# Kernel tuning notes

Hardware: AMD Instinct MI355X
Metric: run time of the kernel (lower is better)

## Reference

```python
import jax, jax.numpy as jnp
import numpy as np

NUM_CLASSES = 2
TOP_K = 200
CONF_THRESH = 0.01
NMS_THRESH = 0.45
VAR0, VAR1 = 0.1, 0.2
NUM_PRIORS = 72192
BATCH = 64


def setup_inputs() -> dict:
    key = jax.random.key(0)
    k1, k2, k3 = jax.random.split(key, 3)
    loc_data = jax.random.normal(k1, (BATCH, NUM_PRIORS, 4), dtype=jnp.float32)
    conf_data = jax.random.uniform(k2, (BATCH * NUM_PRIORS, NUM_CLASSES), dtype=jnp.float32)
    prior_data = jax.random.uniform(k3, (NUM_PRIORS, 4), dtype=jnp.float32) * 0.5 + 0.01
    return {"loc_data": loc_data, "conf_data": conf_data, "prior_data": prior_data}


def decode(loc, priors):
    # loc, priors: [P, 4] (cx, cy, w, h) -> corners (x1, y1, x2, y2)
    cxcy = priors[:, :2] + loc[:, :2] * VAR0 * priors[:, 2:]
    wh = priors[:, 2:] * jnp.exp(loc[:, 2:] * VAR1)
    return jnp.concatenate([cxcy - wh / 2, cxcy + wh / 2], axis=-1)


def pairwise_iou(boxes):
    # boxes: [K, 4] corners
    area = (boxes[:, 2] - boxes[:, 0]) * (boxes[:, 3] - boxes[:, 1])
    lt = jnp.maximum(boxes[:, None, :2], boxes[None, :, :2])
    rb = jnp.minimum(boxes[:, None, 2:], boxes[None, :, 2:])
    wh = jnp.clip(rb - lt, 0.0)
    inter = wh[..., 0] * wh[..., 1]
    union = area[:, None] + area[None, :] - inter
    return inter / jnp.maximum(union, 1e-12)


def nms_single(boxes, scores):
    # boxes: [P,4], scores: [P] -> [TOP_K, 5] rows (score, x1, y1, x2, y2)
    masked = jnp.where(scores > CONF_THRESH, scores, -jnp.inf)
    top_scores, idx = jax.lax.top_k(masked, TOP_K)      # descending, like torch nms
    cand_boxes = boxes[idx]                              # [K,4]
    valid = top_scores > CONF_THRESH
    iou = pairwise_iou(cand_boxes)                       # [K,K]
    ar = jnp.arange(TOP_K)

    def body(i, keep):
        sup = (iou[i] > NMS_THRESH) & (ar > i)
        return jnp.where(keep[i], keep & ~sup, keep)

    keep = jax.lax.fori_loop(0, TOP_K, body, valid)
    # compact kept detections to the front (matches output[i, cl, :count] = ...)
    pos = jnp.cumsum(keep) - 1
    pos = jnp.where(keep, pos, TOP_K)                    # dropped rows scatter out of range
    rows = jnp.concatenate([top_scores[:, None], cand_boxes], axis=1)
    return jnp.zeros((TOP_K, 5), dtype=boxes.dtype).at[pos].set(rows, mode="drop")


def reference(loc_data, conf_data, prior_data):
    num = loc_data.shape[0]
    num_priors = prior_data.shape[0]
    conf_preds = conf_data.reshape(num, num_priors, NUM_CLASSES)  # [B, P, C]
    decoded = jax.vmap(decode, in_axes=(0, None))(loc_data, prior_data)  # [B, P, 4]
    per_class = []
    # class 0 is background -> zeros (matches torch output init)
    per_class.append(jnp.zeros((num, TOP_K, 5), dtype=loc_data.dtype))
    for cl in range(1, NUM_CLASSES):
        per_class.append(jax.vmap(nms_single)(decoded, conf_preds[:, :, cl]))
    # final rank-based zeroing in torch source is a no-op (fill_ on an advanced-index copy)
    return jnp.stack(per_class, axis=1)  # [B, C, TOP_K, 5]
```

## Files before the change

kernel.cpp:

```cpp
#include <hip/hip_runtime.h>
#include <math.h>

#pragma clang fp contract(off)

#define NUM_PRIORS 72192
#define BATCH      64
#define TOPK       200
#define CONF_TH    0.01f
#define NMS_TH     0.45f
#define NBINS      256
#define SLICES     32
#define ROWS       (NUM_PRIORS / SLICES)
#define Q4         (ROWS / 2)
#define CAPS       64
#define CAP        1024
#define KW         7
#define NMS_NTH    1024

typedef unsigned long long u64;

__device__ __forceinline__ int bin_of(float s) {
    int b = (int)(s * 256.0f);
    return b > 255 ? 255 : b;
}

__global__ __launch_bounds__(256) void histcollect_kernel(const float* __restrict__ conf,
                                                          unsigned short* __restrict__ shist,
                                                          unsigned* __restrict__ scnt,
                                                          u64* __restrict__ cand) {
    __shared__ unsigned lh[4][NBINS];
    __shared__ unsigned lcnt;
    const int b = blockIdx.y, slice = blockIdx.x, tid = threadIdx.x;
    const int wv = tid >> 6;
    for (int i = tid; i < 4 * NBINS; i += 256) ((unsigned*)lh)[i] = 0;
    if (tid == 0) lcnt = 0;
    __syncthreads();
    const float4* c4 = (const float4*)conf;
    const long base4 = (long)b * (NUM_PRIORS / 2) + (long)slice * Q4;
    const int prow0 = slice * ROWS;
    u64* seg = cand + ((long)b * SLICES + slice) * CAPS;

    float4 v0 = c4[base4 + tid];
    float4 v1 = c4[base4 + tid + 256];
    float4 v2 = c4[base4 + tid + 512];
    float4 v3 = c4[base4 + tid + 768];

#define PROC(sv, pidx)                                                          \
    do {                                                                        \
        float s_ = (sv);                                                        \
        if (s_ > CONF_TH) {                                                     \
            int bn = bin_of(s_);                                                \
            atomicAdd(&lh[wv][bn], 1u);                                         \
            if (bn == 255) {                                                    \
                unsigned pos = atomicAdd(&lcnt, 1u);                            \
                if (pos < CAPS)                                                 \
                    seg[pos] = ((u64)__float_as_uint(s_) << 32) |               \
                               (u64)(0xFFFFFFFFu - (unsigned)(pidx));           \
            }                                                                   \
        }                                                                       \
    } while (0)

    PROC(v0.y, prow0 + 2 * tid);
    PROC(v0.w, prow0 + 2 * tid + 1);
    PROC(v1.y, prow0 + 2 * (tid + 256));
    PROC(v1.w, prow0 + 2 * (tid + 256) + 1);
    PROC(v2.y, prow0 + 2 * (tid + 512));
    PROC(v2.w, prow0 + 2 * (tid + 512) + 1);
    PROC(v3.y, prow0 + 2 * (tid + 768));
    PROC(v3.w, prow0 + 2 * (tid + 768) + 1);
    if (tid < Q4 - 1024) {
        float4 vt = c4[base4 + tid + 1024];
        PROC(vt.y, prow0 + 2 * (tid + 1024));
        PROC(vt.w, prow0 + 2 * (tid + 1024) + 1);
    }
#undef PROC
    __syncthreads();
    shist[((long)b * SLICES + slice) * NBINS + tid] =
        (unsigned short)(lh[0][tid] + lh[1][tid] + lh[2][tid] + lh[3][tid]);
    if (tid == 0) {
        unsigned c = lcnt;
        scnt[b * SLICES + slice] = (c < CAPS) ? c : CAPS;
    }
}

__global__ __launch_bounds__(256) void fixup_kernel(const float* __restrict__ conf,
                                                    const unsigned short* __restrict__ shist,
                                                    unsigned* __restrict__ scnt,
                                                    u64* __restrict__ cand) {
    __shared__ unsigned suf[NBINS];
    __shared__ int Tsh;
    __shared__ unsigned lcnt;
    const int b = blockIdx.x, tid = threadIdx.x;
    unsigned acc = 0;
    const unsigned short* hb = shist + (long)b * SLICES * NBINS;
#pragma unroll
    for (int s = 0; s < SLICES; s++) acc += (unsigned)hb[s * NBINS + tid];
    suf[tid] = acc;
    if (tid == 0) Tsh = 0;
    __syncthreads();
    for (int off = 1; off < NBINS; off <<= 1) {
        unsigned v = (tid + off < NBINS) ? suf[tid + off] : 0u;
        __syncthreads();
        suf[tid] += v;
        __syncthreads();
    }
    unsigned s0 = suf[tid];
    unsigned sn = (tid + 1 < NBINS) ? suf[tid + 1] : 0u;
    if (s0 >= TOPK && (tid == NBINS - 1 || sn < TOPK)) Tsh = tid;
    __syncthreads();
    const int T = Tsh;
    if (T == 255) return;

    const float4* c4 = (const float4*)conf;
    for (int s = 0; s < SLICES; s++) {
        __syncthreads();
        if (tid == 0) lcnt = 0;
        __syncthreads();
        const long base4 = (long)b * (NUM_PRIORS / 2) + (long)s * Q4;
        const int prow0 = s * ROWS;
        u64* seg = cand + ((long)b * SLICES + s) * CAPS;
        for (int q = tid; q < Q4; q += 256) {
            float4 v = c4[base4 + q];
            float sy = v.y, sw = v.w;
            if (sy > CONF_TH && bin_of(sy) >= T) {
                unsigned pos = atomicAdd(&lcnt, 1u);
                if (pos < CAPS)
                    seg[pos] = ((u64)__float_as_uint(sy) << 32) |
                               (u64)(0xFFFFFFFFu - (unsigned)(prow0 + 2 * q));
            }
            if (sw > CONF_TH && bin_of(sw) >= T) {
                unsigned pos = atomicAdd(&lcnt, 1u);
                if (pos < CAPS)
                    seg[pos] = ((u64)__float_as_uint(sw) << 32) |
                               (u64)(0xFFFFFFFFu - (unsigned)(prow0 + 2 * q + 1));
            }
        }
        __syncthreads();
        if (tid == 0) {
            unsigned c = lcnt;
            scnt[b * SLICES + s] = (c < CAPS) ? c : CAPS;
        }
    }
}

__global__ __launch_bounds__(NMS_NTH) void nms_kernel(const float* __restrict__ loc,
                           const float* __restrict__ prior,
                           const unsigned* __restrict__ scnt,
                           const u64* __restrict__ cand,
                           float* __restrict__ out) {
    __shared__ u64 keys[CAP];
    __shared__ float4 bbox[224];
    __shared__ float bsc_s[TOPK];
    __shared__ unsigned invR[TOPK][8];
    __shared__ unsigned kw0[8];
    __shared__ unsigned kwF[KW];
    __shared__ unsigned char vld[TOPK];
    __shared__ int soff[SLICES + 1];
    __shared__ int scl[SLICES];
    const int b = blockIdx.x, tid = threadIdx.x;

    if (tid < 64) {
        int s = tid;
        int c = 0;
        if (s < SLICES) {
            unsigned cs = scnt[b * SLICES + s];
            c = (cs < CAPS) ? (int)cs : CAPS;
        }
        int v = c;
#pragma unroll
        for (int d = 1; d < 32; d <<= 1) {
            int o = __shfl_up(v, d);
            if ((int)tid >= d) v += o;
        }
        if (s < SLICES) {
            int P = v - c;
            int off = P > CAP ? CAP : P;
            int rem = CAP - off;
            int cl = c < rem ? c : rem;
            soff[s] = off;
            scl[s] = cl;
            if (s == SLICES - 1) soff[SLICES] = (P + c > CAP) ? CAP : (P + c);
        }
    }
    {
        float* ob = out + (long)b * 2 * TOPK * 5;
        for (int i = tid; i < 2 * TOPK * 5; i += NMS_NTH) ob[i] = 0.f;
    }
    if (tid < 224) {
        bbox[tid] = make_float4(0.f, 0.f, 0.f, 0.f);
        if (tid < TOPK) { bsc_s[tid] = 0.f; vld[tid] = 0; }
    }
    __syncthreads();

    const int n = soff[SLICES];
    const int nn = (n + 15) & ~15;
    for (int pos = tid; pos < SLICES * CAPS; pos += NMS_NTH) {
        int s = pos >> 6, idx = pos & 63;
        if (idx < scl[s])
            keys[soff[s] + idx] = cand[((long)b * SLICES + s) * CAPS + idx];
    }
    for (int i = n + tid; i < nn; i += NMS_NTH) keys[i] = 0ull;
    __syncthreads();

    u64 kc = (tid < n) ? keys[tid] : 0ull;
    int rk = 0;
    if ((int)(tid & ~63u) < n) {
        for (int k = 0; k < nn; k += 16) {
            u64 kb[16];
#pragma unroll
            for (int j = 0; j < 16; j++) kb[j] = keys[k + j];
#pragma unroll
            for (int j = 0; j < 16; j++) rk += (kb[j] > kc) ? 1 : 0;
        }
    }
    if (tid < n && rk < TOPK) {
        u64 key = kc;
        float sc = __uint_as_float((unsigned)(key >> 32));
        unsigned p = 0xFFFFFFFFu - (unsigned)(key & 0xFFFFFFFFull);
        float4 l4 = ((const float4*)loc)[(long)b * NUM_PRIORS + p];
        float4 p4 = ((const float4*)prior)[p];
        float cx = p4.x + (l4.x * 0.1f) * p4.z;
        float cy = p4.y + (l4.y * 0.1f) * p4.w;
        float w_ = p4.z * (float)exp((double)(l4.z * 0.2f));
        float h_ = p4.w * (float)exp((double)(l4.w * 0.2f));
        float x1 = cx - w_ * 0.5f, y1 = cy - h_ * 0.5f;
        float x2 = cx + w_ * 0.5f, y2 = cy + h_ * 0.5f;
        bsc_s[rk] = sc;
        bbox[rk] = make_float4(x1, y1, x2, y2);
        vld[rk] = 1;
    }
    __syncthreads();

    {
        const int q = tid >> 8, i = tid & 255;
        if (i < TOPK) {
            const float4 ib = bbox[i];
            const float iar = (ib.z - ib.x) * (ib.w - ib.y);
#pragma unroll
            for (int wi = 0; wi < 2; wi++) {
                if (wi == 1 && q == 3) break;
                const int w = (wi == 0) ? q : q + 4;
                const int jbase = w * 32;
                unsigned inv = 0xFFFFFFFFu;
#pragma unroll
                for (int g = 0; g < 32; g += 8) {
                    float4 J[8];
#pragma unroll
                    for (int r = 0; r < 8; r++) J[r] = bbox[jbase + g + r];
#pragma unroll
                    for (int r = 0; r < 8; r++) {
                        const int j = jbase + g + r;
                        if (j > i && j < TOPK) {
                            float4 jb = J[r];
                            float jar = (jb.z - jb.x) * (jb.w - jb.y);
                            float ltx = fmaxf(ib.x, jb.x);
                            float lty = fmaxf(ib.y, jb.y);
                            float rbx = fminf(ib.z, jb.z);
                            float rby = fminf(ib.w, jb.w);
                            float wx = fmaxf(rbx - ltx, 0.0f);
                            float wy = fmaxf(rby - lty, 0.0f);
                            float inter = wx * wy;
                            float uni = (iar + jar) - inter;
                            float iou = inter / fmaxf(uni, 1e-12f);
                            if (iou > NMS_TH) inv &= ~(1u << (g + r));
                        }
                    }
                }
                invR[i][w] = inv;
            }
            if (q == 0) invR[i][7] = 0xFFFFFFFFu;
        }
    }
    if (tid >= 224 && tid < 224 + KW) {
        const int w = tid - 224;
        unsigned bits = 0u;
        const int nb = (w == 6) ? 8 : 32;
        for (int t = 0; t < nb; t++)
            bits |= (vld[w * 32 + t] ? 1u : 0u) << t;
        kw0[w] = bits;
    }
    __syncthreads();

    if (tid < 64) {
        unsigned kk[KW];
#pragma unroll
        for (int w = 0; w < KW; w++) kk[w] = kw0[w];
#pragma unroll
        for (int g = 0; g < TOPK; g += 8) {
            uint4 A[8], C[8];
#pragma unroll
            for (int r = 0; r < 8; r++) {
                A[r] = *(const uint4*)&invR[g + r][0];
                C[r] = *(const uint4*)&invR[g + r][4];
            }
#pragma unroll
            for (int r = 0; r < 8; r++) {
                const int i = g + r;
                if ((kk[i >> 5] >> (i & 31)) & 1u) {
                    kk[0] &= A[r].x; kk[1] &= A[r].y; kk[2] &= A[r].z; kk[3] &= A[r].w;
                    kk[4] &= C[r].x; kk[5] &= C[r].y; kk[6] &= C[r].z;
                }
            }
        }
        if (tid == 0) {
            kwF[0] = kk[0]; kwF[1] = kk[1]; kwF[2] = kk[2]; kwF[3] = kk[3];
            kwF[4] = kk[4]; kwF[5] = kk[5]; kwF[6] = kk[6];
        }
    }
    __syncthreads();

    if (tid < TOPK) {
        const int wsel = tid >> 5, bsel = tid & 31;
        if ((kwF[wsel] >> bsel) & 1u) {
            int pos = 0;
#pragma unroll
            for (int w = 0; w < KW; w++) {
                unsigned kw_ = kwF[w];
                if (w < wsel) pos += __popc(kw_);
                else if (w == wsel) pos += __popc(kw_ & ((bsel == 0) ? 0u : (0xFFFFFFFFu >> (32 - bsel))));
            }
            float4 jb = bbox[tid];
            float* o = out + (((long)b * 2 + 1) * TOPK + pos) * 5;
            o[0] = bsc_s[tid];
            o[1] = jb.x;
            o[2] = jb.y;
            o[3] = jb.z;
            o[4] = jb.w;
        }
    }
}

extern "C" void kernel_launch(void* const* d_in, const int* in_sizes, int n_in,
                              void* d_out, int out_size, void* d_ws, size_t ws_size,
                              hipStream_t stream) {
    const float* loc   = (const float*)d_in[0];
    const float* conf  = (const float*)d_in[1];
    const float* prior = (const float*)d_in[2];
    float* out = (float*)d_out;

    char* w = (char*)d_ws;
    unsigned short* shist = (unsigned short*)w;
    unsigned* scnt = (unsigned*)(w + 1048576);
    u64* cand      = (u64*)(w + 1056768);

    histcollect_kernel<<<dim3(SLICES, BATCH), 256, 0, stream>>>(conf, shist, scnt, cand);
    fixup_kernel<<<BATCH, 256, 0, stream>>>(conf, shist, scnt, cand);
    nms_kernel<<<BATCH, NMS_NTH, 0, stream>>>(loc, prior, scnt, cand, out);
}
```

Measured before the change: 41.45 us.

## Drop histogram pass, collect top-bin candidates directly, fold rare fallback into NMS

The first kernel no longer builds per-slice 256-bin histograms. It only collects scores in the top bin, with an uncapped count per slice. The fixup kernel is removed, and its histogram, threshold and recollect logic now runs inside the NMS kernel, only when the top-bin total is below TOPK or a slice overflowed. The valid-mask bitmask is built with shared atomicOr instead of a byte array plus a packing pass. This removes one launch and the shared-memory histogram atomics in the common case. The fallback path inside the NMS kernel is slow and serial per batch if it ever triggers, and the removed invR[i][7] init assumes that word is unused.

After: 38.75 us. 1.07x faster.

```diff
diff --git a/kernel.cpp b/kernel.cpp
--- a/kernel.cpp
+++ b/kernel.cpp
@@ -12,10 +12,12 @@
 #define SLICES     32
 #define ROWS       (NUM_PRIORS / SLICES)
 #define Q4         (ROWS / 2)
+#define QB         (NUM_PRIORS / 2)
 #define CAPS       64
 #define CAP        1024
 #define KW         7
 #define NMS_NTH    1024
+#define B255       0.99609375f
 
 typedef unsigned long long u64;
 
@@ -24,19 +26,15 @@
     return b > 255 ? 255 : b;
 }
 
-__global__ __launch_bounds__(256) void histcollect_kernel(const float* __restrict__ conf,
-                                                          unsigned short* __restrict__ shist,
-                                                          unsigned* __restrict__ scnt,
-                                                          u64* __restrict__ cand) {
-    __shared__ unsigned lh[4][NBINS];
+__global__ __launch_bounds__(256) void collect255_kernel(const float* __restrict__ conf,
+                                                         unsigned* __restrict__ scnt,
+                                                         u64* __restrict__ cand) {
     __shared__ unsigned lcnt;
     const int b = blockIdx.y, slice = blockIdx.x, tid = threadIdx.x;
-    const int wv = tid >> 6;
-    for (int i = tid; i < 4 * NBINS; i += 256) ((unsigned*)lh)[i] = 0;
     if (tid == 0) lcnt = 0;
     __syncthreads();
     const float4* c4 = (const float4*)conf;
-    const long base4 = (long)b * (NUM_PRIORS / 2) + (long)slice * Q4;
+    const long base4 = (long)b * QB + (long)slice * Q4;
     const int prow0 = slice * ROWS;
     u64* seg = cand + ((long)b * SLICES + slice) * CAPS;
 
@@ -45,108 +43,40 @@
     float4 v2 = c4[base4 + tid + 512];
     float4 v3 = c4[base4 + tid + 768];
 
-#define PROC(sv, pidx)                                                          \
+#define P255(sv, pidx)                                                          \
     do {                                                                        \
         float s_ = (sv);                                                        \
-        if (s_ > CONF_TH) {                                                     \
-            int bn = bin_of(s_);                                                \
-            atomicAdd(&lh[wv][bn], 1u);                                         \
-            if (bn == 255) {                                                    \
-                unsigned pos = atomicAdd(&lcnt, 1u);                            \
-                if (pos < CAPS)                                                 \
-                    seg[pos] = ((u64)__float_as_uint(s_) << 32) |               \
-                               (u64)(0xFFFFFFFFu - (unsigned)(pidx));           \
-            }                                                                   \
+        if (s_ >= B255) {                                                       \
+            unsigned pos = atomicAdd(&lcnt, 1u);                                \
+            if (pos < CAPS)                                                     \
+                seg[pos] = ((u64)__float_as_uint(s_) << 32) |                   \
+                           (u64)(0xFFFFFFFFu - (unsigned)(pidx));               \
         }                                                                       \
     } while (0)
 
-    PROC(v0.y, prow0 + 2 * tid);
-    PROC(v0.w, prow0 + 2 * tid + 1);
-    PROC(v1.y, prow0 + 2 * (tid + 256));
-    PROC(v1.w, prow0 + 2 * (tid + 256) + 1);
-    PROC(v2.y, prow0 + 2 * (tid + 512));
-    PROC(v2.w, prow0 + 2 * (tid + 512) + 1);
-    PROC(v3.y, prow0 + 2 * (tid + 768));
-    PROC(v3.w, prow0 + 2 * (tid + 768) + 1);
+    P255(v0.y, prow0 + 2 * tid);
+    P255(v0.w, prow0 + 2 * tid + 1);
+    P255(v1.y, prow0 + 2 * (tid + 256));
+    P255(v1.w, prow0 + 2 * (tid + 256) + 1);
+    P255(v2.y, prow0 + 2 * (tid + 512));
+    P255(v2.w, prow0 + 2 * (tid + 512) + 1);
+    P255(v3.y, prow0 + 2 * (tid + 768));
+    P255(v3.w, prow0 + 2 * (tid + 768) + 1);
     if (tid < Q4 - 1024) {
         float4 vt = c4[base4 + tid + 1024];
-        PROC(vt.y, prow0 + 2 * (tid + 1024));
-        PROC(vt.w, prow0 + 2 * (tid + 1024) + 1);
-    }
-#undef PROC
-    __syncthreads();
-    shist[((long)b * SLICES + slice) * NBINS + tid] =
-        (unsigned short)(lh[0][tid] + lh[1][tid] + lh[2][tid] + lh[3][tid]);
-    if (tid == 0) {
-        unsigned c = lcnt;
-        scnt[b * SLICES + slice] = (c < CAPS) ? c : CAPS;
-    }
-}
-
-__global__ __launch_bounds__(256) void fixup_kernel(const float* __restrict__ conf,
-                                                    const unsigned short* __restrict__ shist,
-                                                    unsigned* __restrict__ scnt,
-                                                    u64* __restrict__ cand) {
-    __shared__ unsigned suf[NBINS];
-    __shared__ int Tsh;
-    __shared__ unsigned lcnt;
-    const int b = blockIdx.x, tid = threadIdx.x;
-    unsigned acc = 0;
-    const unsigned short* hb = shist + (long)b * SLICES * NBINS;
-#pragma unroll
-    for (int s = 0; s < SLICES; s++) acc += (unsigned)hb[s * NBINS + tid];
-    suf[tid] = acc;
-    if (tid == 0) Tsh = 0;
-    __syncthreads();
-    for (int off = 1; off < NBINS; off <<= 1) {
-        unsigned v = (tid + off < NBINS) ? suf[tid + off] : 0u;
-        __syncthreads();
-        suf[tid] += v;
-        __syncthreads();
-    }
-    unsigned s0 = suf[tid];
-    unsigned sn = (tid + 1 < NBINS) ? suf[tid + 1] : 0u;
-    if (s0 >= TOPK && (tid == NBINS - 1 || sn < TOPK)) Tsh = tid;
-    __syncthreads();
-    const int T = Tsh;
-    if (T == 255) return;
-
-    const float4* c4 = (const float4*)conf;
-    for (int s = 0; s < SLICES; s++) {
-        __syncthreads();
-        if (tid == 0) lcnt = 0;
-        __syncthreads();
-        const long base4 = (long)b * (NUM_PRIORS / 2) + (long)s * Q4;
-        const int prow0 = s * ROWS;
-        u64* seg = cand + ((long)b * SLICES + s) * CAPS;
-        for (int q = tid; q < Q4; q += 256) {
-            float4 v = c4[base4 + q];
-            float sy = v.y, sw = v.w;
-            if (sy > CONF_TH && bin_of(sy) >= T) {
-                unsigned pos = atomicAdd(&lcnt, 1u);
-                if (pos < CAPS)
-                    seg[pos] = ((u64)__float_as_uint(sy) << 32) |
-                               (u64)(0xFFFFFFFFu - (unsigned)(prow0 + 2 * q));
-            }
-            if (sw > CONF_TH && bin_of(sw) >= T) {
-                unsigned pos = atomicAdd(&lcnt, 1u);
-                if (pos < CAPS)
-                    seg[pos] = ((u64)__float_as_uint(sw) << 32) |
-                               (u64)(0xFFFFFFFFu - (unsigned)(prow0 + 2 * q + 1));
-            }
-        }
-        __syncthreads();
-        if (tid == 0) {
-            unsigned c = lcnt;
-            scnt[b * SLICES + s] = (c < CAPS) ? c : CAPS;
-        }
-    }
+        P255(vt.y, prow0 + 2 * (tid + 1024));
+        P255(vt.w, prow0 + 2 * (tid + 1024) + 1);
+    }
+#undef P255
+    __syncthreads();
+    if (tid == 0) scnt[b * SLICES + slice] = lcnt;
 }
 
 __global__ __launch_bounds__(NMS_NTH) void nms_kernel(const float* __restrict__ loc,
                            const float* __restrict__ prior,
+                           const float* __restrict__ conf,
                            const unsigned* __restrict__ scnt,
-                           const u64* __restrict__ cand,
+                           u64* __restrict__ cand,
                            float* __restrict__ out) {
     __shared__ u64 keys[CAP];
     __shared__ float4 bbox[224];
@@ -154,24 +84,27 @@
     __shared__ unsigned invR[TOPK][8];
     __shared__ unsigned kw0[8];
     __shared__ unsigned kwF[KW];
-    __shared__ unsigned char vld[TOPK];
     __shared__ int soff[SLICES + 1];
     __shared__ int scl[SLICES];
+    __shared__ unsigned histc[NBINS];
+    __shared__ unsigned lcnt32[SLICES];
+    __shared__ int TshC, needfix;
     const int b = blockIdx.x, tid = threadIdx.x;
 
     if (tid < 64) {
         int s = tid;
-        int c = 0;
-        if (s < SLICES) {
-            unsigned cs = scnt[b * SLICES + s];
-            c = (cs < CAPS) ? (int)cs : CAPS;
-        }
+        unsigned cs = (s < SLICES) ? scnt[b * SLICES + s] : 0u;
+        int c = (cs < CAPS) ? (int)cs : CAPS;
         int v = c;
 #pragma unroll
         for (int d = 1; d < 32; d <<= 1) {
             int o = __shfl_up(v, d);
             if ((int)tid >= d) v += o;
         }
+        unsigned tot = cs;
+#pragma unroll
+        for (int d = 32; d >= 1; d >>= 1) tot += __shfl_xor(tot, d);
+        u64 ovb = __ballot(cs > CAPS);
         if (s < SLICES) {
             int P = v - c;
             int off = P > CAP ? CAP : P;
@@ -181,16 +114,83 @@
             scl[s] = cl;
             if (s == SLICES - 1) soff[SLICES] = (P + c > CAP) ? CAP : (P + c);
         }
+        if (tid == 0) {
+            needfix = (tot < TOPK) || (ovb != 0ull);
+            TshC = 0;
+        }
     }
     {
         float* ob = out + (long)b * 2 * TOPK * 5;
         for (int i = tid; i < 2 * TOPK * 5; i += NMS_NTH) ob[i] = 0.f;
     }
-    if (tid < 224) {
-        bbox[tid] = make_float4(0.f, 0.f, 0.f, 0.f);
-        if (tid < TOPK) { bsc_s[tid] = 0.f; vld[tid] = 0; }
-    }
-    __syncthreads();
+    if (tid < 8) kw0[tid] = 0u;
+    __syncthreads();
+
+    if (needfix) {
+        const float4* c4 = (const float4*)conf;
+        for (int i = tid; i < NBINS; i += NMS_NTH) histc[i] = 0u;
+        __syncthreads();
+        for (int q = tid; q < QB; q += NMS_NTH) {
+            float4 v = c4[(long)b * QB + q];
+            if (v.y > CONF_TH) atomicAdd(&histc[bin_of(v.y)], 1u);
+            if (v.w > CONF_TH) atomicAdd(&histc[bin_of(v.w)], 1u);
+        }
+        __syncthreads();
+        for (int off = 1; off < NBINS; off <<= 1) {
+            unsigned vv = 0u;
+            if (tid < NBINS && tid + off < NBINS) vv = histc[tid + off];
+            __syncthreads();
+            if (tid < NBINS) histc[tid] += vv;
+            __syncthreads();
+        }
+        if (tid < NBINS) {
+            unsigned s0 = histc[tid];
+            unsigned sn = (tid + 1 < NBINS) ? histc[tid + 1] : 0u;
+            if (s0 >= TOPK && (tid == NBINS - 1 || sn < TOPK)) TshC = tid;
+        }
+        if (tid < SLICES) lcnt32[tid] = 0u;
+        __syncthreads();
+        const int T = TshC;
+        for (int q = tid; q < QB; q += NMS_NTH) {
+            float4 v = c4[(long)b * QB + q];
+            int sl = q / Q4;
+            u64* seg = cand + ((long)b * SLICES + sl) * CAPS;
+            if (v.y > CONF_TH && bin_of(v.y) >= T) {
+                unsigned pos = atomicAdd(&lcnt32[sl], 1u);
+                if (pos < CAPS)
+                    seg[pos] = ((u64)__float_as_uint(v.y) << 32) |
+                               (u64)(0xFFFFFFFFu - (unsigned)(2 * q));
+            }
+            if (v.w > CONF_TH && bin_of(v.w) >= T) {
+                unsigned pos = atomicAdd(&lcnt32[sl], 1u);
+                if (pos < CAPS)
+                    seg[pos] = ((u64)__float_as_uint(v.w) << 32) |
+                               (u64)(0xFFFFFFFFu - (unsigned)(2 * q + 1));
+            }
+        }
+        __syncthreads();
+        if (tid < 64) {
+            int s = tid;
+            unsigned cs = (s < SLICES) ? lcnt32[s] : 0u;
+            int c = (cs < CAPS) ? (int)cs : CAPS;
+            int v = c;
+#pragma unroll
+            for (int d = 1; d < 32; d <<= 1) {
+                int o = __shfl_up(v, d);
+                if ((int)tid >= d) v += o;
+            }
+            if (s < SLICES) {
+                int P = v - c;
+                int off = P > CAP ? CAP : P;
+                int rem = CAP - off;
+                int cl = c < rem ? c : rem;
+                soff[s] = off;
+                scl[s] = cl;
+                if (s == SLICES - 1) soff[SLICES] = (P + c > CAP) ? CAP : (P + c);
+            }
+        }
+        __syncthreads();
+    }
 
     const int n = soff[SLICES];
     const int nn = (n + 15) & ~15;
@@ -227,7 +227,7 @@
         float x2 = cx + w_ * 0.5f, y2 = cy + h_ * 0.5f;
         bsc_s[rk] = sc;
         bbox[rk] = make_float4(x1, y1, x2, y2);
-        vld[rk] = 1;
+        atomicOr(&kw0[rk >> 5], 1u << (rk & 31));
     }
     __syncthreads();
 
@@ -268,16 +268,7 @@
                 }
                 invR[i][w] = inv;
             }
-            if (q == 0) invR[i][7] = 0xFFFFFFFFu;
-        }
-    }
-    if (tid >= 224 && tid < 224 + KW) {
-        const int w = tid - 224;
-        unsigned bits = 0u;
-        const int nb = (w == 6) ? 8 : 32;
-        for (int t = 0; t < nb; t++)
-            bits |= (vld[w * 32 + t] ? 1u : 0u) << t;
-        kw0[w] = bits;
+        }
     }
     __syncthreads();
 
@@ -339,11 +330,9 @@
     float* out = (float*)d_out;
 
     char* w = (char*)d_ws;
-    unsigned short* shist = (unsigned short*)w;
-    unsigned* scnt = (unsigned*)(w + 1048576);
-    u64* cand      = (u64*)(w + 1056768);
-
-    histcollect_kernel<<<dim3(SLICES, BATCH), 256, 0, stream>>>(conf, shist, scnt, cand);
-    fixup_kernel<<<BATCH, 256, 0, stream>>>(conf, shist, scnt, cand);
-    nms_kernel<<<BATCH, NMS_NTH, 0, stream>>>(loc, prior, scnt, cand, out);
+    unsigned* scnt = (unsigned*)w;
+    u64* cand      = (u64*)(w + 8192);
+
+    collect255_kernel<<<dim3(SLICES, BATCH), 256, 0, stream>>>(conf, scnt, cand);
+    nms_kernel<<<BATCH, NMS_NTH, 0, stream>>>(loc, prior, conf, scnt, cand, out);
 }
```
